# Kernel optimization log

Measured on AMD Instinct MI355X. Metric: run time of the kernel, lower is better.

The kernel has to match this reference:

```python
import jax, jax.numpy as jnp
import numpy as np
from jax import lax

DN = ('NCHW', 'OIHW', 'NCHW')

def conv2d(x, w, b, pad):
    y = lax.conv_general_dilated(x, w, (1, 1), [(pad, pad), (pad, pad)], dimension_numbers=DN)
    return y + b[None, :, None, None]

def setup_inputs() -> dict:
    key = jax.random.key(0)
    ks = jax.random.split(key, 12)
    B, H, W, C, K = 32, 256, 256, 16, 32
    x = jax.random.normal(ks[0], (B, 1, H, W), jnp.float32)
    s = 0.1
    stem_w = jax.random.normal(ks[1], (C, 1, 3, 3), jnp.float32) * s
    stem_b = jnp.zeros((C,), jnp.float32)
    up1_w = jax.random.normal(ks[2], (C, C, 3, 3), jnp.float32) * s
    up1_b = jnp.zeros((C,), jnp.float32)
    up2_w = jax.random.normal(ks[3], (C, C, 1, 1), jnp.float32) * s
    up2_b = jnp.zeros((C,), jnp.float32)
    tau_w = jax.random.normal(ks[4], (C, C, 1, 1), jnp.float32) * s
    tau_b = jnp.zeros((C,), jnp.float32)
    codebook = jax.random.uniform(ks[5], (K, C), jnp.float32, -1.0 / K, 1.0 / K)
    dec_w = jax.random.normal(ks[6], (1, C, 1, 1), jnp.float32) * s
    dec_b = jnp.zeros((1,), jnp.float32)
    return {"x": x, "stem_w": stem_w, "stem_b": stem_b, "up1_w": up1_w, "up1_b": up1_b,
            "up2_w": up2_w, "up2_b": up2_b, "tau_w": tau_w, "tau_b": tau_b,
            "codebook": codebook, "dec_w": dec_w, "dec_b": dec_b, "n_steps": 5}

def vq(z, codebook):
    # z: [B,C,H,W], codebook: [K,C]
    B, C, H, W = z.shape
    K = codebook.shape[0]
    z_flat = jnp.transpose(z, (0, 2, 3, 1)).reshape(-1, C)  # [N,C]
    dists = (jnp.sum(z_flat ** 2, axis=1, keepdims=True)
             + jnp.sum(codebook ** 2, axis=1)
             - 2.0 * z_flat @ codebook.T)  # [N,K]
    indices = jnp.argmin(dists, axis=1)  # [N]
    z_q = jnp.transpose(codebook[indices].reshape(B, H, W, C), (0, 3, 1, 2))
    commit_loss = jnp.mean((lax.stop_gradient(z_q) - z) ** 2)
    codebook_loss = jnp.mean((z_q - lax.stop_gradient(z)) ** 2)
    vq_loss = codebook_loss + 0.25 * commit_loss
    z_q_st = z + lax.stop_gradient(z_q - z)
    used = jnp.zeros((K,), jnp.float32).at[indices].set(1.0)
    usage = jnp.sum(used) / K
    return z_q_st, vq_loss, usage, indices.reshape(B, H, W)

def reference(x, stem_w, stem_b, up1_w, up1_b, up2_w, up2_b, tau_w, tau_b, codebook, dec_w, dec_b, n_steps):
    state = jax.nn.relu(conv2d(x, stem_w, stem_b, 1))
    vq_total = jnp.float32(0.0)
    usage_total = jnp.float32(0.0)
    for _ in range(n_steps):
        delta = conv2d(jax.nn.relu(conv2d(state, up1_w, up1_b, 1)), up2_w, up2_b, 0)
        beta = jax.nn.sigmoid(conv2d(state, tau_w, tau_b, 0))
        state = beta * state + (1.0 - beta) * delta
        state, vq_loss, usage, _ = vq(state, codebook)
        vq_total = vq_total + vq_loss
        usage_total = usage_total + usage
    output = jax.nn.sigmoid(conv2d(state, dec_w, dec_b, 0))
    return output, vq_total / n_steps, usage_total / n_steps
```

## Files before the change

kernel.cpp:

```cpp
#include <hip/hip_runtime.h>
#include <math.h>

#define DEV __device__ __forceinline__

namespace {
constexpr int B_ = 32, H_ = 256, W_ = 256;
constexpr size_t NPIX = (size_t)B_ * H_ * W_;

constexpr int QT9 = 0;
constexpr int QAB = 5940;
constexpr int QCB = 7220;
constexpr int QU2 = 7860;
constexpr int QTOT = 8116;
constexpr int QLDS = 7220;

constexpr int IW1 = 0;
constexpr int IU2 = 2304;
constexpr int ITA = 2560;
constexpr int ICB = 2816;
constexpr int IB1 = 3456;
constexpr int IB2 = 3472;
constexpr int ITB = 3488;
constexpr int ISB = 3504;
constexpr int ISW = 3520;
constexpr int ITOT = 3664;

constexpr size_t OFF_QTAB = 2 * NPIX;
constexpr size_t OFF_ITAB = OFF_QTAB + (size_t)QTOT * 4;
constexpr size_t OFF_DLUT = OFF_ITAB + (size_t)ITOT * 4;
constexpr size_t OFF_LOSS = (OFF_DLUT + 128 + 7) & ~(size_t)7;
constexpr size_t OFF_MASK = OFF_LOSS + 5 * 8;
}

typedef float f2v __attribute__((ext_vector_type(2)));

struct V16 { f2v h[8]; };

DEV f2v fma2(f2v a, f2v b, f2v c) {
#if __has_builtin(__builtin_elementwise_fma)
    return __builtin_elementwise_fma(a, b, c);
#else
    f2v r; r.x = fmaf(a.x, b.x, c.x); r.y = fmaf(a.y, b.y, c.y); return r;
#endif
}
DEV f2v max2(f2v a, f2v b) {
#if __has_builtin(__builtin_elementwise_max)
    return __builtin_elementwise_max(a, b);
#else
    f2v r; r.x = fmaxf(a.x, b.x); r.y = fmaxf(a.y, b.y); return r;
#endif
}

DEV V16 v16z() {
    V16 r;
    #pragma unroll
    for (int j = 0; j < 8; ++j) r.h[j] = (f2v){0.f, 0.f};
    return r;
}
DEV void v16fma(V16& a, const V16& w, float s) {
    f2v ss = (f2v){s, s};
    #pragma unroll
    for (int j = 0; j < 8; ++j) a.h[j] = fma2(w.h[j], ss, a.h[j]);
}
DEV void v16add(V16& a, const V16& b) {
    #pragma unroll
    for (int j = 0; j < 8; ++j) a.h[j] = a.h[j] + b.h[j];
}
DEV void v16relu(V16& a) {
    f2v z = (f2v){0.f, 0.f};
    #pragma unroll
    for (int j = 0; j < 8; ++j) a.h[j] = max2(a.h[j], z);
}
DEV float v16dot(const V16& a, const V16& b) {
    f2v acc = (f2v){0.f, 0.f};
    #pragma unroll
    for (int j = 0; j < 8; ++j) acc = fma2(a.h[j], b.h[j], acc);
    return acc.x + acc.y;
}
DEV V16 ld16(const float* p) {
    const float4* q = (const float4*)p;
    float4 A = q[0], Bv = q[1], C = q[2], D = q[3];
    V16 r;
    r.h[0] = (f2v){A.x, A.y};  r.h[1] = (f2v){A.z, A.w};
    r.h[2] = (f2v){Bv.x, Bv.y}; r.h[3] = (f2v){Bv.z, Bv.w};
    r.h[4] = (f2v){C.x, C.y};  r.h[5] = (f2v){C.z, C.w};
    r.h[6] = (f2v){D.x, D.y};  r.h[7] = (f2v){D.z, D.w};
    return r;
}
DEV void st16(float* p, const V16& v) {
    float4* q = (float4*)p;
    q[0] = make_float4(v.h[0].x, v.h[0].y, v.h[1].x, v.h[1].y);
    q[1] = make_float4(v.h[2].x, v.h[2].y, v.h[3].x, v.h[3].y);
    q[2] = make_float4(v.h[4].x, v.h[4].y, v.h[5].x, v.h[5].y);
    q[3] = make_float4(v.h[6].x, v.h[6].y, v.h[7].x, v.h[7].y);
}
DEV void v16sig(V16& a) {
    #pragma unroll
    for (int j = 0; j < 8; ++j) {
        a.h[j].x = 1.f / (1.f + expf(-a.h[j].x));
        a.h[j].y = 1.f / (1.f + expf(-a.h[j].y));
    }
}

__global__ void k_setup(const float* __restrict__ w1, const float* __restrict__ b1,
                        const float* __restrict__ u2w, const float* __restrict__ b2,
                        const float* __restrict__ tw, const float* __restrict__ tb,
                        const float* __restrict__ cb, const float* __restrict__ stw,
                        const float* __restrict__ stb, const float* __restrict__ dw,
                        const float* __restrict__ db,
                        float* __restrict__ gQ, float* __restrict__ gI,
                        float* __restrict__ dlut, double* __restrict__ lossS,
                        unsigned int* __restrict__ maskS)
{
    int tid = threadIdx.x;
    if (tid < 5) { lossS[tid] = 0.0; maskS[tid] = 0u; }
    for (int e = tid; e < 297; e += 256) {
        int t = e / 33, k = e % 33;
        float* dst = &gQ[QT9 + e * 20];
        for (int o = 0; o < 16; ++o) {
            float acc = 0.f;
            if (k < 32) {
                for (int i = 0; i < 16; ++i)
                    acc = fmaf(w1[o * 144 + i * 9 + t], cb[k * 16 + i], acc);
                if (t == 4) acc += b1[o];
            }
            dst[o] = acc;
        }
        dst[16] = dst[17] = dst[18] = dst[19] = 0.f;
    }
    if (tid < 32) {
        int k = tid;
        float nrm = 0.f;
        for (int c = 0; c < 16; ++c) { float v = cb[k * 16 + c]; nrm = fmaf(v, v, nrm); }
        for (int c = 0; c < 16; ++c) { gQ[QCB + k * 20 + c] = cb[k * 16 + c]; gI[ICB + k * 20 + c] = cb[k * 16 + c]; }
        gQ[QCB + k * 20 + 16] = nrm; gI[ICB + k * 20 + 16] = nrm;
        for (int c = 17; c < 20; ++c) { gQ[QCB + k * 20 + c] = 0.f; gI[ICB + k * 20 + c] = 0.f; }
        float dacc = db[0];
        for (int c = 0; c < 16; ++c) dacc = fmaf(dw[c], cb[k * 16 + c], dacc);
        dlut[k] = 1.f / (1.f + expf(-dacc));
        for (int c = 0; c < 16; ++c) {
            float ta = tb[c];
            for (int i = 0; i < 16; ++i) ta = fmaf(tw[c * 16 + i], cb[k * 16 + i], ta);
            float beta = 1.f / (1.f + expf(-ta));
            gQ[QAB + k * 20 + c] = beta * cb[k * 16 + c] + (1.f - beta) * b2[c];
            gQ[QAB + (32 + k) * 20 + c] = 1.f - beta;
        }
        for (int c = 16; c < 20; ++c) { gQ[QAB + k * 20 + c] = 0.f; gQ[QAB + (32 + k) * 20 + c] = 0.f; }
    }
    if (tid < 16) {
        int i = tid;
        for (int o = 0; o < 16; ++o) {
            gQ[QU2 + i * 16 + o] = u2w[o * 16 + i];
            gI[IU2 + i * 16 + o] = u2w[o * 16 + i];
            gI[ITA + i * 16 + o] = tw[o * 16 + i];
        }
        gI[IB1 + i] = b1[i]; gI[IB2 + i] = b2[i]; gI[ITB + i] = tb[i]; gI[ISB + i] = stb[i];
    }
    for (int e = tid; e < 144; e += 256) {
        int t = e / 16, i = e % 16;
        float* dst = &gI[IW1 + e * 16];
        for (int o = 0; o < 16; ++o) dst[o] = w1[o * 144 + i * 9 + t];
    }
    if (tid < 9) {
        int t = tid;
        for (int o = 0; o < 16; ++o) gI[ISW + t * 16 + o] = stw[o * 9 + t];
    }
}

__global__ __launch_bounds__(256, 3) void k_iter1(
    const float* __restrict__ x, const float* __restrict__ gI,
    unsigned char* __restrict__ idx_out, double* __restrict__ lossS,
    unsigned int* __restrict__ maskS)
{
    __shared__ __align__(16) float xt[20 * 36];
    __shared__ __align__(16) float stE[306 * 20];
    __shared__ __align__(16) float stO[306 * 20];
    __shared__ double dsum[4];
    __shared__ unsigned int msum[4];
    const int lx = threadIdx.x, ly = threadIdx.y;
    const int lid = ly * 16 + lx;
    const int b = blockIdx.z, oy = blockIdx.y * 16, ox = blockIdx.x * 32;
    const float* xb = x + (size_t)b * (H_ * W_);
    for (int i = lid; i < 720; i += 256) {
        int iy = i / 36, ix = i % 36;
        int gy = oy - 2 + iy, gx = ox - 2 + ix;
        float v = 0.f;
        if ((unsigned)gy < (unsigned)H_ && (unsigned)gx < (unsigned)W_) v = xb[gy * W_ + gx];
        xt[i] = v;
    }
    __syncthreads();
    for (int q = lid; q < 612; q += 256) {
        int sy = q / 34, sx = q % 34;
        int gy = oy - 1 + sy, gx = ox - 1 + sx;
        bool inb = ((unsigned)gy < (unsigned)H_ && (unsigned)gx < (unsigned)W_);
        V16 a = ld16(&gI[ISB]);
        #pragma unroll
        for (int t = 0; t < 9; ++t) {
            float xv = xt[(sy + t / 3) * 36 + sx + t % 3];
            V16 w = ld16(&gI[ISW + t * 16]);
            v16fma(a, w, xv);
        }
        v16relu(a);
        if (!inb) a = v16z();
        float* dst = ((sx & 1) ? stO : stE) + (sy * 17 + (sx >> 1)) * 20;
        st16(dst, a);
    }
    __syncthreads();
    V16 u0 = ld16(&gI[IB1]);
    V16 u1 = u0;
    #pragma unroll
    for (int t = 0; t < 9; ++t) {
        const int r = ly + t / 3, dx = t % 3;
        const float* p0; const float* p1;
        if (dx == 0)      { p0 = &stE[(r * 17 + lx) * 20];     p1 = &stO[(r * 17 + lx) * 20]; }
        else if (dx == 1) { p0 = &stO[(r * 17 + lx) * 20];     p1 = &stE[(r * 17 + lx + 1) * 20]; }
        else              { p0 = &stE[(r * 17 + lx + 1) * 20]; p1 = &stO[(r * 17 + lx + 1) * 20]; }
        V16 s0 = ld16(p0), s1 = ld16(p1);
        const int base = IW1 + t * 256;
        #pragma unroll
        for (int j = 0; j < 8; ++j) {
            f2v a0 = s0.h[j], a1 = s1.h[j];
            V16 wA = ld16(&gI[base + (2 * j) * 16]);
            v16fma(u0, wA, a0.x); v16fma(u1, wA, a1.x);
            V16 wB = ld16(&gI[base + (2 * j + 1) * 16]);
            v16fma(u0, wB, a0.y); v16fma(u1, wB, a1.y);
        }
    }
    v16relu(u0); v16relu(u1);
    V16 c0 = ld16(&stO[((ly + 1) * 17 + lx) * 20]);
    V16 c1 = ld16(&stE[((ly + 1) * 17 + lx + 1) * 20]);
    V16 v0 = ld16(&gI[IB2]);
    V16 v1 = v0;
    #pragma unroll
    for (int j = 0; j < 8; ++j) {
        f2v a0 = u0.h[j], a1 = u1.h[j];
        V16 wA = ld16(&gI[IU2 + (2 * j) * 16]);
        v16fma(v0, wA, a0.x); v16fma(v1, wA, a1.x);
        V16 wB = ld16(&gI[IU2 + (2 * j + 1) * 16]);
        v16fma(v0, wB, a0.y); v16fma(v1, wB, a1.y);
    }
    V16 t0 = ld16(&gI[ITB]);
    V16 t1 = t0;
    #pragma unroll
    for (int j = 0; j < 8; ++j) {
        f2v a0 = c0.h[j], a1 = c1.h[j];
        V16 wA = ld16(&gI[ITA + (2 * j) * 16]);
        v16fma(t0, wA, a0.x); v16fma(t1, wA, a1.x);
        V16 wB = ld16(&gI[ITA + (2 * j + 1) * 16]);
        v16fma(t0, wB, a0.y); v16fma(t1, wB, a1.y);
    }
    v16sig(t0); v16sig(t1);
    V16 z0, z1;
    #pragma unroll
    for (int j = 0; j < 8; ++j) {
        z0.h[j] = fma2(t0.h[j], c0.h[j] - v0.h[j], v0.h[j]);
        z1.h[j] = fma2(t1.h[j], c1.h[j] - v1.h[j], v1.h[j]);
    }
    float zz0 = v16dot(z0, z0), zz1 = v16dot(z1, z1);
    float best0 = 3.4e38f, best1 = 3.4e38f; int bk0 = 0, bk1 = 0;
    #pragma unroll 4
    for (int k = 0; k < 32; ++k) {
        V16 q = ld16(&gI[ICB + k * 20]);
        float cn = gI[ICB + k * 20 + 16];
        float d0 = (zz0 + cn) - 2.0f * v16dot(q, z0);
        float d1 = (zz1 + cn) - 2.0f * v16dot(q, z1);
        if (d0 < best0) { best0 = d0; bk0 = k; }
        if (d1 < best1) { best1 = d1; bk1 = k; }
    }
    unsigned short pr = (unsigned short)(bk0 | (bk1 << 8));
    *(unsigned short*)(idx_out + (size_t)b * (H_ * W_) + (size_t)(oy + ly) * W_ + ox + 2 * lx) = pr;
    float lp = best0 + best1;
    unsigned int m = (1u << bk0) | (1u << bk1);
    #pragma unroll
    for (int off = 32; off > 0; off >>= 1) {
        lp += __shfl_down(lp, off, 64);
        m |= __shfl_down(m, off, 64);
    }
    if ((lid & 63) == 0) { dsum[lid >> 6] = (double)lp; msum[lid >> 6] = m; }
    __syncthreads();
    if (lid == 0) {
        atomicAdd(lossS, dsum[0] + dsum[1] + dsum[2] + dsum[3]);
        atomicOr(maskS, msum[0] | msum[1] | msum[2] | msum[3]);
    }
}

__global__ __launch_bounds__(256, 3) void k_qstep(
    const unsigned char* __restrict__ idx_in, unsigned char* __restrict__ idx_out,
    const float* __restrict__ gQ, double* __restrict__ lossS,
    unsigned int* __restrict__ maskS, float* __restrict__ out_px,
    const float* __restrict__ dlut)
{
    __shared__ __align__(16) float tab[QLDS];
    __shared__ unsigned char ct[18 * 80];
    __shared__ float lut[32];
    __shared__ double dsum[4];
    __shared__ unsigned int msum[4];
    const int tx = threadIdx.x, ty = threadIdx.y;
    const int lid = ty * 16 + tx;
    const int b = blockIdx.z, oy = blockIdx.y * 16, ox = blockIdx.x * 64;
    for (int i = lid; i < QLDS / 4; i += 256) ((float4*)tab)[i] = ((const float4*)gQ)[i];
    if (lid < 32) lut[lid] = dlut[lid];
    const unsigned char* ib = idx_in + (size_t)b * (H_ * W_);
    for (int i = lid; i < 18 * 66; i += 256) {
        int r = i / 66, c = i % 66;
        int gy = oy - 1 + r, gx = ox - 1 + c;
        unsigned char v = 32;
        if ((unsigned)gy < (unsigned)H_ && (unsigned)gx < (unsigned)W_) v = ib[gy * W_ + gx];
        ct[r * 80 + c] = v;
    }
    __syncthreads();
    const int cx = tx * 4;
    int K[3][6];
    #pragma unroll
    for (int r = 0; r < 3; ++r) {
        unsigned int w0 = *(const unsigned int*)&ct[(ty + r) * 80 + cx];
        unsigned int w1 = *(const unsigned int*)&ct[(ty + r) * 80 + cx + 4];
        K[r][0] = w0 & 255; K[r][1] = (w0 >> 8) & 255; K[r][2] = (w0 >> 16) & 255;
        K[r][3] = w0 >> 24; K[r][4] = w1 & 255; K[r][5] = (w1 >> 8) & 255;
    }
    V16 V[4];
    #pragma unroll
    for (int half = 0; half < 2; ++half) {
        const int p0 = half * 2, p1 = half * 2 + 1;
        V16 U0 = v16z(), U1 = v16z();
        #pragma unroll
        for (int t = 0; t < 9; ++t) {
            const int dy = t / 3, dx = t % 3;
            V16 e0 = ld16(&tab[(t * 33 + K[dy][p0 + dx]) * 20]);
            v16add(U0, e0);
            V16 e1 = ld16(&tab[(t * 33 + K[dy][p1 + dx]) * 20]);
            v16add(U1, e1);
        }
        v16relu(U0); v16relu(U1);
        V16 v0 = v16z(), v1 = v16z();
        #pragma unroll
        for (int j = 0; j < 8; ++j) {
            f2v a0 = U0.h[j], a1 = U1.h[j];
            V16 wA = ld16(&gQ[QU2 + (2 * j) * 16]);
            v16fma(v0, wA, a0.x); v16fma(v1, wA, a1.x);
            V16 wB = ld16(&gQ[QU2 + (2 * j + 1) * 16]);
            v16fma(v0, wB, a0.y); v16fma(v1, wB, a1.y);
        }
        {
            int kc = K[1][p0 + 1];
            V16 a = ld16(&tab[QAB + kc * 20]);
            V16 bb = ld16(&tab[QAB + (32 + kc) * 20]);
            #pragma unroll
            for (int j = 0; j < 8; ++j) v0.h[j] = fma2(bb.h[j], v0.h[j], a.h[j]);
        }
        {
            int kc = K[1][p1 + 1];
            V16 a = ld16(&tab[QAB + kc * 20]);
            V16 bb = ld16(&tab[QAB + (32 + kc) * 20]);
            #pragma unroll
            for (int j = 0; j < 8; ++j) v1.h[j] = fma2(bb.h[j], v1.h[j], a.h[j]);
        }
        V[p0] = v0; V[p1] = v1;
    }
    float zz[4], best[4]; int bk[4];
    #pragma unroll
    for (int p = 0; p < 4; ++p) { zz[p] = v16dot(V[p], V[p]); best[p] = 3.4e38f; bk[p] = 0; }
    #pragma unroll 4
    for (int k = 0; k < 32; ++k) {
        V16 q = ld16(&gQ[QCB + k * 20]);
        float cn = gQ[QCB + k * 20 + 16];
        #pragma unroll
        for (int p = 0; p < 4; ++p) {
            float d = (zz[p] + cn) - 2.0f * v16dot(q, V[p]);
            if (d < best[p]) { best[p] = d; bk[p] = k; }
        }
    }
    const size_t pofs = (size_t)b * (H_ * W_) + (size_t)(oy + ty) * W_ + ox + cx;
    if (out_px) {
        float4 o4 = make_float4(lut[bk[0]], lut[bk[1]], lut[bk[2]], lut[bk[3]]);
        *(float4*)(out_px + pofs) = o4;
    } else {
        unsigned int pack = (unsigned)bk[0] | ((unsigned)bk[1] << 8) |
                            ((unsigned)bk[2] << 16) | ((unsigned)bk[3] << 24);
        *(unsigned int*)(idx_out + pofs) = pack;
    }
    float lp = best[0] + best[1] + best[2] + best[3];
    unsigned int m = (1u << bk[0]) | (1u << bk[1]) | (1u << bk[2]) | (1u << bk[3]);
    #pragma unroll
    for (int off = 32; off > 0; off >>= 1) {
        lp += __shfl_down(lp, off, 64);
        m |= __shfl_down(m, off, 64);
    }
    if ((lid & 63) == 0) { dsum[lid >> 6] = (double)lp; msum[lid >> 6] = m; }
    __syncthreads();
    if (lid == 0) {
        atomicAdd(lossS, dsum[0] + dsum[1] + dsum[2] + dsum[3]);
        atomicOr(maskS, msum[0] | msum[1] | msum[2] | msum[3]);
    }
}

__global__ void k_scalars(float* __restrict__ out, const double* __restrict__ lossS,
                          const unsigned int* __restrict__ maskS)
{
    if (threadIdx.x == 0) {
        double vq = 0.0; float us = 0.f;
        for (int s = 0; s < 5; ++s) {
            vq += 1.25 * lossS[s] / 33554432.0;
            us += (float)__popc(maskS[s]) / 32.0f;
        }
        out[NPIX] = (float)(vq / 5.0);
        out[NPIX + 1] = us / 5.0f;
    }
}

extern "C" void kernel_launch(void* const* d_in, const int* in_sizes, int n_in,
                              void* d_out, int out_size, void* d_ws, size_t ws_size,
                              hipStream_t stream)
{
    const float* x   = (const float*)d_in[0];
    const float* stw = (const float*)d_in[1];
    const float* stb = (const float*)d_in[2];
    const float* w1  = (const float*)d_in[3];
    const float* b1  = (const float*)d_in[4];
    const float* u2w = (const float*)d_in[5];
    const float* b2  = (const float*)d_in[6];
    const float* tw  = (const float*)d_in[7];
    const float* tb  = (const float*)d_in[8];
    const float* cb  = (const float*)d_in[9];
    const float* dw  = (const float*)d_in[10];
    const float* db  = (const float*)d_in[11];

    char* ws = (char*)d_ws;
    unsigned char* idxA = (unsigned char*)ws;
    unsigned char* idxB = (unsigned char*)(ws + NPIX);
    float* gQ   = (float*)(ws + OFF_QTAB);
    float* gI   = (float*)(ws + OFF_ITAB);
    float* dlut = (float*)(ws + OFF_DLUT);
    double* lossS = (double*)(ws + OFF_LOSS);
    unsigned int* maskS = (unsigned int*)(ws + OFF_MASK);

    dim3 blk(16, 16, 1);
    dim3 g1(W_ / 32, H_ / 16, B_);
    dim3 gq(W_ / 64, H_ / 16, B_);
    float* out = (float*)d_out;
    k_setup<<<1, 256, 0, stream>>>(w1, b1, u2w, b2, tw, tb, cb, stw, stb, dw, db,
                                   gQ, gI, dlut, lossS, maskS);
    k_iter1<<<g1, blk, 0, stream>>>(x, gI, idxA, lossS + 0, maskS + 0);
    k_qstep<<<gq, blk, 0, stream>>>(idxA, idxB, gQ, lossS + 1, maskS + 1, nullptr, dlut);
    k_qstep<<<gq, blk, 0, stream>>>(idxB, idxA, gQ, lossS + 2, maskS + 2, nullptr, dlut);
    k_qstep<<<gq, blk, 0, stream>>>(idxA, idxB, gQ, lossS + 3, maskS + 3, nullptr, dlut);
    k_qstep<<<gq, blk, 0, stream>>>(idxB, idxA, gQ, lossS + 4, maskS + 4, out, dlut);
    k_scalars<<<1, 64, 0, stream>>>(out, lossS, maskS);
}
```

Measured before the change: 615.5 us.

## Fuse pairs of quantized steps into one kernel with halo recompute

Two consecutive VQ update steps now run in one kernel. The first step is computed over a tile enlarged by a one-pixel halo, and its results are kept in shared memory as codebook indices that feed the second step. This halves the number of launches and the global index reads and writes between steps, at the cost of recomputing the halo: 18x130 pixels are computed for every 16x128 tile, plus extra LDS use. The setup kernel is also spread over 16 blocks so its per-output work runs in parallel, and launch bounds rise to 4 blocks per CU.

```diff
diff --git a/kernel.cpp b/kernel.cpp
--- a/kernel.cpp
+++ b/kernel.cpp
@@ -102,6 +102,63 @@
     }
 }
 
+DEV void group4(const float* tab, const float* __restrict__ gQ,
+                const int K[3][6], int bk[4], float best[4])
+{
+    V16 V[4];
+    #pragma unroll
+    for (int half = 0; half < 2; ++half) {
+        const int p0 = half * 2, p1 = half * 2 + 1;
+        V16 U0 = v16z(), U1 = v16z();
+        #pragma unroll
+        for (int t = 0; t < 9; ++t) {
+            const int dy = t / 3, dx = t % 3;
+            V16 e0 = ld16(&tab[(t * 33 + K[dy][p0 + dx]) * 20]);
+            v16add(U0, e0);
+            V16 e1 = ld16(&tab[(t * 33 + K[dy][p1 + dx]) * 20]);
+            v16add(U1, e1);
+        }
+        v16relu(U0); v16relu(U1);
+        V16 v0 = v16z(), v1 = v16z();
+        #pragma unroll
+        for (int j = 0; j < 8; ++j) {
+            f2v a0 = U0.h[j], a1 = U1.h[j];
+            V16 wA = ld16(&gQ[QU2 + (2 * j) * 16]);
+            v16fma(v0, wA, a0.x); v16fma(v1, wA, a1.x);
+            V16 wB = ld16(&gQ[QU2 + (2 * j + 1) * 16]);
+            v16fma(v0, wB, a0.y); v16fma(v1, wB, a1.y);
+        }
+        {
+            int kc = K[1][p0 + 1];
+            V16 a = ld16(&tab[QAB + kc * 20]);
+            V16 bb = ld16(&tab[QAB + (32 + kc) * 20]);
+            #pragma unroll
+            for (int j = 0; j < 8; ++j) v0.h[j] = fma2(bb.h[j], v0.h[j], a.h[j]);
+        }
+        {
+            int kc = K[1][p1 + 1];
+            V16 a = ld16(&tab[QAB + kc * 20]);
+            V16 bb = ld16(&tab[QAB + (32 + kc) * 20]);
+            #pragma unroll
+            for (int j = 0; j < 8; ++j) v1.h[j] = fma2(bb.h[j], v1.h[j], a.h[j]);
+        }
+        V[p0] = v0; V[p1] = v1;
+    }
+    float zz[4];
+    #pragma unroll
+    for (int p = 0; p < 4; ++p) { zz[p] = v16dot(V[p], V[p]); best[p] = 3.4e38f; bk[p] = 0; }
+    #pragma unroll 4
+    for (int k = 0; k < 32; ++k) {
+        V16 q = ld16(&gQ[QCB + k * 20]);
+        float cn = gQ[QCB + k * 20 + 16];
+        #pragma unroll
+        for (int p = 0; p < 4; ++p) {
+            float d = (zz[p] + cn) - 2.0f * v16dot(q, V[p]);
+            if (d < best[p]) { best[p] = d; bk[p] = k; }
+        }
+    }
+}
+
 __global__ void k_setup(const float* __restrict__ w1, const float* __restrict__ b1,
                         const float* __restrict__ u2w, const float* __restrict__ b2,
                         const float* __restrict__ tw, const float* __restrict__ tb,
@@ -112,22 +169,30 @@
                         float* __restrict__ dlut, double* __restrict__ lossS,
                         unsigned int* __restrict__ maskS)
 {
-    int tid = threadIdx.x;
-    if (tid < 5) { lossS[tid] = 0.0; maskS[tid] = 0u; }
-    for (int e = tid; e < 297; e += 256) {
+    const int tid = threadIdx.x;
+    const int gtid = blockIdx.x * 256 + tid;
+    if (gtid < 5) { lossS[gtid] = 0.0; maskS[gtid] = 0u; }
+    for (int p = gtid; p < 297 * 16; p += 4096) {
+        int e = p >> 4, o = p & 15;
         int t = e / 33, k = e % 33;
-        float* dst = &gQ[QT9 + e * 20];
-        for (int o = 0; o < 16; ++o) {
-            float acc = 0.f;
-            if (k < 32) {
-                for (int i = 0; i < 16; ++i)
-                    acc = fmaf(w1[o * 144 + i * 9 + t], cb[k * 16 + i], acc);
-                if (t == 4) acc += b1[o];
-            }
-            dst[o] = acc;
-        }
-        dst[16] = dst[17] = dst[18] = dst[19] = 0.f;
-    }
+        float acc = 0.f;
+        if (k < 32) {
+            for (int i = 0; i < 16; ++i)
+                acc = fmaf(w1[o * 144 + i * 9 + t], cb[k * 16 + i], acc);
+            if (t == 4) acc += b1[o];
+        }
+        gQ[QT9 + e * 20 + o] = acc;
+    }
+    for (int e = gtid; e < 297; e += 4096) {
+        gQ[QT9 + e * 20 + 16] = 0.f; gQ[QT9 + e * 20 + 17] = 0.f;
+        gQ[QT9 + e * 20 + 18] = 0.f; gQ[QT9 + e * 20 + 19] = 0.f;
+    }
+    for (int p = gtid; p < 144 * 16; p += 4096) {
+        int e = p >> 4, o = p & 15;
+        int t = e / 16, i = e % 16;
+        gI[IW1 + e * 16 + o] = w1[o * 144 + i * 9 + t];
+    }
+    if (blockIdx.x != 0) return;
     if (tid < 32) {
         int k = tid;
         float nrm = 0.f;
@@ -155,11 +220,6 @@
             gI[ITA + i * 16 + o] = tw[o * 16 + i];
         }
         gI[IB1 + i] = b1[i]; gI[IB2 + i] = b2[i]; gI[ITB + i] = tb[i]; gI[ISB + i] = stb[i];
-    }
-    for (int e = tid; e < 144; e += 256) {
-        int t = e / 16, i = e % 16;
-        float* dst = &gI[IW1 + e * 16];
-        for (int o = 0; o < 16; ++o) dst[o] = w1[o * 144 + i * 9 + t];
     }
     if (tid < 9) {
         int t = tid;
@@ -284,113 +344,111 @@
     }
 }
 
-__global__ __launch_bounds__(256, 3) void k_qstep(
+__global__ __launch_bounds__(256, 4) void k_qstep2(
     const unsigned char* __restrict__ idx_in, unsigned char* __restrict__ idx_out,
-    const float* __restrict__ gQ, double* __restrict__ lossS,
-    unsigned int* __restrict__ maskS, float* __restrict__ out_px,
-    const float* __restrict__ dlut)
+    const float* __restrict__ gQ,
+    double* __restrict__ lossA, unsigned int* __restrict__ maskA,
+    double* __restrict__ lossB, unsigned int* __restrict__ maskB,
+    float* __restrict__ out_px, const float* __restrict__ dlut)
 {
     __shared__ __align__(16) float tab[QLDS];
-    __shared__ unsigned char ct[18 * 80];
+    __shared__ unsigned char ctA[20 * 144];
+    __shared__ unsigned char ctB[18 * 144];
     __shared__ float lut[32];
-    __shared__ double dsum[4];
-    __shared__ unsigned int msum[4];
+    __shared__ double dsA[4], dsB[4];
+    __shared__ unsigned int msA[4], msB[4];
     const int tx = threadIdx.x, ty = threadIdx.y;
     const int lid = ty * 16 + tx;
-    const int b = blockIdx.z, oy = blockIdx.y * 16, ox = blockIdx.x * 64;
+    const int b = blockIdx.z, oy = blockIdx.y * 16, ox = blockIdx.x * 128;
     for (int i = lid; i < QLDS / 4; i += 256) ((float4*)tab)[i] = ((const float4*)gQ)[i];
     if (lid < 32) lut[lid] = dlut[lid];
     const unsigned char* ib = idx_in + (size_t)b * (H_ * W_);
-    for (int i = lid; i < 18 * 66; i += 256) {
-        int r = i / 66, c = i % 66;
-        int gy = oy - 1 + r, gx = ox - 1 + c;
+    for (int i = lid; i < 20 * 136; i += 256) {
+        int r = i / 136, c = i % 136;
+        int gy = oy - 2 + r, gx = ox - 2 + c;
         unsigned char v = 32;
         if ((unsigned)gy < (unsigned)H_ && (unsigned)gx < (unsigned)W_) v = ib[gy * W_ + gx];
-        ct[r * 80 + c] = v;
+        ctA[r * 144 + c] = v;
     }
     __syncthreads();
-    const int cx = tx * 4;
-    int K[3][6];
+    float lpA = 0.f; unsigned int mA = 0u;
+    for (int g = lid; g < 594; g += 256) {
+        int rr = g / 33, c0 = (g % 33) * 4;
+        int K[3][6];
+        #pragma unroll
+        for (int r = 0; r < 3; ++r) {
+            unsigned int w0 = *(const unsigned int*)&ctA[(rr + r) * 144 + c0];
+            unsigned int w1 = *(const unsigned int*)&ctA[(rr + r) * 144 + c0 + 4];
+            K[r][0] = w0 & 255; K[r][1] = (w0 >> 8) & 255; K[r][2] = (w0 >> 16) & 255;
+            K[r][3] = w0 >> 24; K[r][4] = w1 & 255; K[r][5] = (w1 >> 8) & 255;
+        }
+        int bk[4]; float best[4];
+        group4(tab, gQ, K, bk, best);
+        unsigned int pack = 0;
+        #pragma unroll
+        for (int p = 0; p < 4; ++p) {
+            int cc = c0 + p;
+            int gy = oy - 1 + rr, gx = ox - 1 + cc;
+            bool valid = ((unsigned)gy < (unsigned)H_) && ((unsigned)gx < (unsigned)W_) && (cc < 130);
+            unsigned int byte = valid ? (unsigned int)bk[p] : 32u;
+            pack |= byte << (8 * p);
+            bool owned = (rr >= 1) && (rr <= 16) && (cc >= 1) && (cc <= 128);
+            if (owned) { lpA += best[p]; mA |= 1u << bk[p]; }
+        }
+        *(unsigned int*)&ctB[rr * 144 + c0] = pack;
+    }
+    __syncthreads();
+    const int cx = tx * 8;
+    int K10[3][10];
     #pragma unroll
     for (int r = 0; r < 3; ++r) {
-        unsigned int w0 = *(const unsigned int*)&ct[(ty + r) * 80 + cx];
-        unsigned int w1 = *(const unsigned int*)&ct[(ty + r) * 80 + cx + 4];
-        K[r][0] = w0 & 255; K[r][1] = (w0 >> 8) & 255; K[r][2] = (w0 >> 16) & 255;
-        K[r][3] = w0 >> 24; K[r][4] = w1 & 255; K[r][5] = (w1 >> 8) & 255;
-    }
-    V16 V[4];
-    #pragma unroll
-    for (int half = 0; half < 2; ++half) {
-        const int p0 = half * 2, p1 = half * 2 + 1;
-        V16 U0 = v16z(), U1 = v16z();
-        #pragma unroll
-        for (int t = 0; t < 9; ++t) {
-            const int dy = t / 3, dx = t % 3;
-            V16 e0 = ld16(&tab[(t * 33 + K[dy][p0 + dx]) * 20]);
-            v16add(U0, e0);
-            V16 e1 = ld16(&tab[(t * 33 + K[dy][p1 + dx]) * 20]);
-            v16add(U1, e1);
-        }
-        v16relu(U0); v16relu(U1);
-        V16 v0 = v16z(), v1 = v16z();
-        #pragma unroll
-        for (int j = 0; j < 8; ++j) {
-            f2v a0 = U0.h[j], a1 = U1.h[j];
-            V16 wA = ld16(&gQ[QU2 + (2 * j) * 16]);
-            v16fma(v0, wA, a0.x); v16fma(v1, wA, a1.x);
-            V16 wB = ld16(&gQ[QU2 + (2 * j + 1) * 16]);
-            v16fma(v0, wB, a0.y); v16fma(v1, wB, a1.y);
-        }
-        {
-            int kc = K[1][p0 + 1];
-            V16 a = ld16(&tab[QAB + kc * 20]);
-            V16 bb = ld16(&tab[QAB + (32 + kc) * 20]);
+        unsigned int w0 = *(const unsigned int*)&ctB[(ty + r) * 144 + cx];
+        unsigned int w1 = *(const unsigned int*)&ctB[(ty + r) * 144 + cx + 4];
+        unsigned int w2 = *(const unsigned int*)&ctB[(ty + r) * 144 + cx + 8];
+        K10[r][0] = w0 & 255; K10[r][1] = (w0 >> 8) & 255; K10[r][2] = (w0 >> 16) & 255; K10[r][3] = w0 >> 24;
+        K10[r][4] = w1 & 255; K10[r][5] = (w1 >> 8) & 255; K10[r][6] = (w1 >> 16) & 255; K10[r][7] = w1 >> 24;
+        K10[r][8] = w2 & 255; K10[r][9] = (w2 >> 8) & 255;
+    }
+    float lpB = 0.f; unsigned int mB = 0u;
+    #pragma unroll
+    for (int g = 0; g < 2; ++g) {
+        const int gofs = g * 4;
+        int K[3][6];
+        #pragma unroll
+        for (int r = 0; r < 3; ++r)
             #pragma unroll
-            for (int j = 0; j < 8; ++j) v0.h[j] = fma2(bb.h[j], v0.h[j], a.h[j]);
-        }
-        {
-            int kc = K[1][p1 + 1];
-            V16 a = ld16(&tab[QAB + kc * 20]);
-            V16 bb = ld16(&tab[QAB + (32 + kc) * 20]);
-            #pragma unroll
-            for (int j = 0; j < 8; ++j) v1.h[j] = fma2(bb.h[j], v1.h[j], a.h[j]);
-        }
-        V[p0] = v0; V[p1] = v1;
-    }
-    float zz[4], best[4]; int bk[4];
-    #pragma unroll
-    for (int p = 0; p < 4; ++p) { zz[p] = v16dot(V[p], V[p]); best[p] = 3.4e38f; bk[p] = 0; }
-    #pragma unroll 4
-    for (int k = 0; k < 32; ++k) {
-        V16 q = ld16(&gQ[QCB + k * 20]);
-        float cn = gQ[QCB + k * 20 + 16];
-        #pragma unroll
-        for (int p = 0; p < 4; ++p) {
-            float d = (zz[p] + cn) - 2.0f * v16dot(q, V[p]);
-            if (d < best[p]) { best[p] = d; bk[p] = k; }
-        }
-    }
-    const size_t pofs = (size_t)b * (H_ * W_) + (size_t)(oy + ty) * W_ + ox + cx;
-    if (out_px) {
-        float4 o4 = make_float4(lut[bk[0]], lut[bk[1]], lut[bk[2]], lut[bk[3]]);
-        *(float4*)(out_px + pofs) = o4;
-    } else {
-        unsigned int pack = (unsigned)bk[0] | ((unsigned)bk[1] << 8) |
-                            ((unsigned)bk[2] << 16) | ((unsigned)bk[3] << 24);
-        *(unsigned int*)(idx_out + pofs) = pack;
-    }
-    float lp = best[0] + best[1] + best[2] + best[3];
-    unsigned int m = (1u << bk[0]) | (1u << bk[1]) | (1u << bk[2]) | (1u << bk[3]);
+            for (int j = 0; j < 6; ++j) K[r][j] = K10[r][gofs + j];
+        int bk[4]; float best[4];
+        group4(tab, gQ, K, bk, best);
+        const size_t pofs = (size_t)b * (H_ * W_) + (size_t)(oy + ty) * W_ + ox + cx + gofs;
+        if (out_px) {
+            float4 o4 = make_float4(lut[bk[0]], lut[bk[1]], lut[bk[2]], lut[bk[3]]);
+            *(float4*)(out_px + pofs) = o4;
+        } else {
+            unsigned int pack = (unsigned)bk[0] | ((unsigned)bk[1] << 8) |
+                                ((unsigned)bk[2] << 16) | ((unsigned)bk[3] << 24);
+            *(unsigned int*)(idx_out + pofs) = pack;
+        }
+        lpB += best[0] + best[1] + best[2] + best[3];
+        mB |= (1u << bk[0]) | (1u << bk[1]) | (1u << bk[2]) | (1u << bk[3]);
+    }
     #pragma unroll
     for (int off = 32; off > 0; off >>= 1) {
-        lp += __shfl_down(lp, off, 64);
-        m |= __shfl_down(m, off, 64);
-    }
-    if ((lid & 63) == 0) { dsum[lid >> 6] = (double)lp; msum[lid >> 6] = m; }
+        lpA += __shfl_down(lpA, off, 64);
+        mA |= __shfl_down(mA, off, 64);
+        lpB += __shfl_down(lpB, off, 64);
+        mB |= __shfl_down(mB, off, 64);
+    }
+    if ((lid & 63) == 0) {
+        dsA[lid >> 6] = (double)lpA; msA[lid >> 6] = mA;
+        dsB[lid >> 6] = (double)lpB; msB[lid >> 6] = mB;
+    }
     __syncthreads();
     if (lid == 0) {
-        atomicAdd(lossS, dsum[0] + dsum[1] + dsum[2] + dsum[3]);
-        atomicOr(maskS, msum[0] | msum[1] | msum[2] | msum[3]);
+        atomicAdd(lossA, dsA[0] + dsA[1] + dsA[2] + dsA[3]);
+        atomicOr(maskA, msA[0] | msA[1] | msA[2] | msA[3]);
+        atomicAdd(lossB, dsB[0] + dsB[1] + dsB[2] + dsB[3]);
+        atomicOr(maskB, msB[0] | msB[1] | msB[2] | msB[3]);
     }
 }
 
@@ -436,14 +494,14 @@
 
     dim3 blk(16, 16, 1);
     dim3 g1(W_ / 32, H_ / 16, B_);
-    dim3 gq(W_ / 64, H_ / 16, B_);
+    dim3 gq(W_ / 128, H_ / 16, B_);
     float* out = (float*)d_out;
-    k_setup<<<1, 256, 0, stream>>>(w1, b1, u2w, b2, tw, tb, cb, stw, stb, dw, db,
-                                   gQ, gI, dlut, lossS, maskS);
+    k_setup<<<16, 256, 0, stream>>>(w1, b1, u2w, b2, tw, tb, cb, stw, stb, dw, db,
+                                    gQ, gI, dlut, lossS, maskS);
     k_iter1<<<g1, blk, 0, stream>>>(x, gI, idxA, lossS + 0, maskS + 0);
-    k_qstep<<<gq, blk, 0, stream>>>(idxA, idxB, gQ, lossS + 1, maskS + 1, nullptr, dlut);
-    k_qstep<<<gq, blk, 0, stream>>>(idxB, idxA, gQ, lossS + 2, maskS + 2, nullptr, dlut);
-    k_qstep<<<gq, blk, 0, stream>>>(idxA, idxB, gQ, lossS + 3, maskS + 3, nullptr, dlut);
-    k_qstep<<<gq, blk, 0, stream>>>(idxB, idxA, gQ, lossS + 4, maskS + 4, out, dlut);
+    k_qstep2<<<gq, blk, 0, stream>>>(idxA, idxB, gQ, lossS + 1, maskS + 1,
+                                     lossS + 2, maskS + 2, nullptr, dlut);
+    k_qstep2<<<gq, blk, 0, stream>>>(idxB, idxA, gQ, lossS + 3, maskS + 3,
+                                     lossS + 4, maskS + 4, out, dlut);
     k_scalars<<<1, 64, 0, stream>>>(out, lossS, maskS);
 }
```

Result: faster. 550.9 us (-10.5%).
